# Kernel tuning notes

Measured on AMD Instinct MI355X. Metric: run time of the kernel, lower is better.

## Reference

```python
import jax, jax.numpy as jnp
import numpy as np

N = 50000          # number of nodes / output rows (len(degs))
IN_C, OUT_C = 16, 16
EDGE_F = 13        # edge feature dim fed to filter net
HID = 32           # filter-net hidden width
E_NOMINAL = 800000 # target number of edges (sum of degs)


def setup_inputs() -> dict:
    rng = np.random.default_rng(0)
    # variable per-node degrees in [0, 32], adjusted so they sum exactly to E_NOMINAL
    degs = rng.integers(0, 33, size=N).astype(np.int64)
    degs[0] = max(0, degs[0] + (E_NOMINAL - int(degs.sum())))
    E = int(degs.sum())
    # segment id of each edge = destination node (equivalent to the degs-driven loop)
    idxd = np.repeat(np.arange(N, dtype=np.int32), degs)
    idxn = rng.integers(0, N, size=E).astype(np.int32)  # source node gather index

    key = jax.random.key(0)
    k1, k2, k3, k4 = jax.random.split(key, 4)
    x = jax.random.normal(k1, (N, IN_C), jnp.float32)
    edgefeats = jax.random.normal(k2, (E, EDGE_F), jnp.float32)
    # filter net: Linear(EDGE_F->HID) -> ReLU -> Linear(HID->IN_C*OUT_C)
    W1 = jax.random.normal(k3, (EDGE_F, HID), jnp.float32) / np.float32(np.sqrt(EDGE_F))
    b1 = jnp.zeros((HID,), jnp.float32)
    W2 = jax.random.normal(k4, (HID, IN_C * OUT_C), jnp.float32) / np.float32(np.sqrt(HID))
    b2 = jnp.zeros((IN_C * OUT_C,), jnp.float32)
    return {
        "x": x, "edgefeats": edgefeats,
        "W1": W1, "b1": b1, "W2": W2, "b2": b2,
        "idxn": jnp.asarray(idxn), "idxd": jnp.asarray(idxd),
        "degs": jnp.asarray(degs.astype(np.float32)),
    }


def reference(x, edgefeats, W1, b1, W2, b2, idxn, idxd, degs):
    # filter net generates a per-edge [IN_C, OUT_C] weight matrix
    h = jax.nn.relu(edgefeats @ W1 + b1)                 # [E, HID]
    w = (h @ W2 + b2).reshape(-1, IN_C, OUT_C)           # [E, IN_C, OUT_C]
    # gather source-node features and apply per-edge matvec (bmm with [E,1,IN_C])
    sel = x[idxn]                                        # [E, IN_C]
    prod = jnp.einsum('ei,eio->eo', sel, w)              # [E, OUT_C]
    # segment-mean over each node's incoming edges; degree-0 nodes -> 0
    s = jax.ops.segment_sum(prod, idxd, num_segments=N)  # [N, OUT_C]
    d = degs[:, None]
    return jnp.where(d > 0, s / jnp.maximum(d, 1.0), jnp.float32(0.0))
```

## Files before the change

kernel.cpp:

```cpp
#include <hip/hip_runtime.h>

typedef _Float16 half2v __attribute__((ext_vector_type(2)));
typedef _Float16 half4v __attribute__((ext_vector_type(4)));
typedef _Float16 half8v __attribute__((ext_vector_type(8)));
typedef float   float4v __attribute__((ext_vector_type(4)));

#define INC     16
#define OUTC    16
#define EFN     13
#define HIDC    32
#define EPB     128
#define MAXSPAN 80

union H8 { half8v v; half2v h2[4]; };

__global__ __launch_bounds__(256) void prep(
    const float* __restrict__ W2,
    const float* __restrict__ x,
    _Float16*    __restrict__ wsB,
    _Float16*    __restrict__ wsXh,
    int nh)
{
    const int b = blockIdx.x;
    if (b < 32) {
        const int i = b * 256 + threadIdx.x;
        const int j = i & 7;
        const int l = (i >> 3) & 63;
        const int t = i >> 9;
        const int q = l >> 4, n = l & 15;
        const int kk = (j < 4) ? (q * 4 + j) : (16 + q * 4 + (j & 3));
        wsB[i] = (_Float16)W2[kk * 256 + t * 16 + n];
    } else {
        const int i = (b - 32) * 256 + threadIdx.x;
        if (i * 8 < nh) {
            const float4 v0 = ((const float4*)x)[i * 2];
            const float4 v1 = ((const float4*)x)[i * 2 + 1];
            half8v h;
            h[0] = (_Float16)v0.x; h[1] = (_Float16)v0.y;
            h[2] = (_Float16)v0.z; h[3] = (_Float16)v0.w;
            h[4] = (_Float16)v1.x; h[5] = (_Float16)v1.y;
            h[6] = (_Float16)v1.z; h[7] = (_Float16)v1.w;
            *(half8v*)(wsXh + (size_t)i * 8) = h;
        }
    }
}

__global__ __launch_bounds__(64, 4) void edge_kernel(
    const _Float16* __restrict__ xh,
    const float* __restrict__ edgefeats,
    const float* __restrict__ W1,
    const float* __restrict__ b1,
    const float* __restrict__ b2,
    const int*   __restrict__ idxn,
    const int*   __restrict__ idxd,
    const float* __restrict__ degs,
    const _Float16* __restrict__ wsB,
    float*       __restrict__ out,
    float*       __restrict__ wsPfirst,
    float*       __restrict__ wsPlast,
    int*         __restrict__ wsMeta,
    int E)
{
    __shared__ float lacc[MAXSPAN * OUTC];
    __shared__ __align__(4) unsigned char su[EPB];

    const int lane = threadIdx.x;
    const int n    = lane & 15;
    const int q    = lane >> 4;

    const long b0   = (long)blockIdx.x * EPB;
    const long bEnd = (b0 + EPB < (long)E) ? (b0 + EPB) : (long)E;
    const int  d_lo = idxd[b0];
    const int  d_hi = idxd[bEnd - 1];
    const int  span = d_hi - d_lo;

    H8 bfr[16];
    #pragma unroll
    for (int t = 0; t < 16; ++t)
        bfr[t].v = *(const half8v*)(wsB + ((size_t)(t * 64 + lane) * 8));

    #pragma unroll
    for (int it = 0; it < MAXSPAN * OUTC / 64; ++it) lacc[lane + it * 64] = 0.0f;
    {
        const int i2 = lane * 2;
        long e0 = b0 + i2, e1 = b0 + i2 + 1;
        if (e0 >= (long)E) e0 = E - 1;
        if (e1 >= (long)E) e1 = E - 1;
        const unsigned u0 = (unsigned)(idxd[e0] - d_lo);
        const unsigned u1 = (unsigned)(idxd[e1] - d_lo);
        *(unsigned short*)&su[i2] = (unsigned short)(u0 | (u1 << 8));
    }

    half4v a1, a2;
    float4v c1, c2;
    #pragma unroll
    for (int jj = 0; jj < 4; ++jj) {
        const int f = q * 4 + jj;
        const bool ok = (f < EFN);
        a1[jj] = ok ? (_Float16)W1[f * HIDC + n]      : (_Float16)0.f;
        a2[jj] = ok ? (_Float16)W1[f * HIDC + 16 + n] : (_Float16)0.f;
        c1[jj] = b1[q * 4 + jj];
        c2[jj] = b1[16 + q * 4 + jj];
    }
    half8v bfragB2;
    #pragma unroll
    for (int j = 0; j < 8; ++j) {
        _Float16 val = (_Float16)0.f;
        if (q < 2) val = (_Float16)b2[(q * 8 + j) * 16 + n];
        bfragB2[j] = val;
    }

    const int f0 = (q < 3) ? (q * 4) : 9;

    __syncthreads();

    const int ntile_blk = (int)((bEnd - b0 + 15) >> 4);

    const long Em1 = (long)E - 1;
    long e0n = b0 + n;
    const int node0 = idxn[(e0n < (long)E) ? e0n : Em1];
    int nodeN = idxn[(e0n + 16 < (long)E) ? (e0n + 16) : Em1];
    half8v xA = *(const half8v*)(xh + (size_t)node0 * INC);
    half8v xB = *(const half8v*)(xh + (size_t)node0 * INC + 8);
    long ec0 = (e0n < (long)E) ? e0n : Em1;
    float4 efc = *(const float4*)(edgefeats + (size_t)ec0 * EFN + f0);

    for (int t16 = 0; t16 < ntile_blk; ++t16) {
        const long base = b0 + (long)t16 * 16;
        const bool vM   = (base + n < (long)E);

        const long en2 = base + 32 + n;
        const int nodeN2 = idxn[(en2 < (long)E) ? en2 : Em1];
        const half8v xA1 = *(const half8v*)(xh + (size_t)nodeN * INC);
        const half8v xB1 = *(const half8v*)(xh + (size_t)nodeN * INC + 8);
        const long en1 = base + 16 + n;
        const long en1c = (en1 < (long)E) ? en1 : Em1;
        const float4 ef1 = *(const float4*)(edgefeats + (size_t)en1c * EFN + f0);

        const unsigned u4 = *(const unsigned*)&su[t16 * 16 + q * 4];

        H8 sa, sb_;
        sa.v = xA; sb_.v = xB;
        const half2v zz = {(_Float16)0.f, (_Float16)0.f};
        half2v selh[8];
        #pragma unroll
        for (int i = 0; i < 4; ++i) {
            selh[i]     = vM ? sa.h2[i]  : zz;
            selh[4 + i] = vM ? sb_.h2[i] : zz;
        }

        half4v efB;
        if (q < 3) {
            efB[0] = (_Float16)efc.x; efB[1] = (_Float16)efc.y;
            efB[2] = (_Float16)efc.z; efB[3] = (_Float16)efc.w;
        } else {
            efB[0] = (_Float16)efc.w; efB[1] = (_Float16)0.f;
            efB[2] = (_Float16)0.f;   efB[3] = (_Float16)0.f;
        }

        const float4v hf1 = __builtin_amdgcn_mfma_f32_16x16x16f16(a1, efB, c1, 0, 0, 0);
        const float4v hf2 = __builtin_amdgcn_mfma_f32_16x16x16f16(a2, efB, c2, 0, 0, 0);

        H8 hu;
        #pragma unroll
        for (int r = 0; r < 2; ++r) {
            half2v t1 = {(_Float16)fmaxf(hf1[2*r], 0.f), (_Float16)fmaxf(hf1[2*r+1], 0.f)};
            half2v t2 = {(_Float16)fmaxf(hf2[2*r], 0.f), (_Float16)fmaxf(hf2[2*r+1], 0.f)};
            hu.h2[r]     = t1;
            hu.h2[2 + r] = t2;
        }

        float4v acc = {0.f, 0.f, 0.f, 0.f};
        #pragma unroll
        for (int t = 0; t < 16; ++t) {
            _Float16 sv = (t & 1) ? selh[t >> 1][1] : selh[t >> 1][0];
            half2v sb = {sv, sv};
            H8 a;
            a.h2[0] = sb * hu.h2[0];
            a.h2[1] = sb * hu.h2[1];
            a.h2[2] = sb * hu.h2[2];
            a.h2[3] = sb * hu.h2[3];
            acc = __builtin_amdgcn_mfma_f32_16x16x32_f16(a.v, bfr[t].v, acc, 0, 0, 0);
        }
        {
            H8 a;
            #pragma unroll
            for (int j2 = 0; j2 < 4; ++j2) {
                a.h2[j2] = (q < 2) ? selh[q * 4 + j2] : zz;
            }
            acc = __builtin_amdgcn_mfma_f32_16x16x32_f16(a.v, bfragB2, acc, 0, 0, 0);
        }

        const unsigned rep = (u4 & 0xffu) * 0x01010101u;
        if (u4 == rep) {
            atomicAdd(&lacc[(u4 & 0xffu) * OUTC + n],
                      acc[0] + acc[1] + acc[2] + acc[3]);
        } else {
            #pragma unroll
            for (int r = 0; r < 4; ++r)
                atomicAdd(&lacc[((u4 >> (8 * r)) & 0xffu) * OUTC + n], acc[r]);
        }

        nodeN = nodeN2;
        xA = xA1; xB = xB1;
        efc = ef1;
    }

    __syncthreads();

    const bool first_starts = (b0 == 0)        || (idxd[b0 - 1] != d_lo);
    const bool last_ends    = (bEnd == (long)E) || (idxd[bEnd]   != d_hi);

    for (int i = lane; i < (span + 1) * OUTC; i += 64) {
        const int u = i >> 4;
        const int o = i & 15;
        const int v = d_lo + u;
        const float bin = lacc[u * OUTC + o];
        const bool starts = (u > 0)    || first_starts;
        const bool ends   = (u < span) || last_ends;
        if (starts && ends) {
            const float dg = degs[v];
            out[(size_t)v * OUTC + o] = (dg > 0.0f) ? bin / dg : 0.0f;
        } else if (!starts) {
            wsPfirst[(size_t)blockIdx.x * OUTC + o] = bin;
        } else {
            wsPlast[(size_t)blockIdx.x * OUTC + o] = bin;
        }
    }
    if (lane == 0) {
        wsMeta[blockIdx.x * 4 + 0] = d_hi;
        wsMeta[blockIdx.x * 4 + 1] = last_ends ? 1 : 0;
        wsMeta[blockIdx.x * 4 + 2] =
            (((span > 0) || first_starts) && !last_ends) ? 1 : 0;
    }
}

__global__ __launch_bounds__(256) void fixup_kernel(
    const float* __restrict__ degs,
    float*       __restrict__ out,
    const float* __restrict__ wsPfirst,
    const float* __restrict__ wsPlast,
    const int*   __restrict__ wsMeta,
    int N, int nblocks)
{
    const int t = blockIdx.x * 256 + threadIdx.x;

    if (t < nblocks && wsMeta[t * 4 + 2]) {
        const int v = wsMeta[t * 4 + 0];
        float tot[OUTC];
        #pragma unroll
        for (int o = 0; o < OUTC; ++o) tot[o] = wsPlast[(size_t)t * OUTC + o];
        for (int j = t + 1; j < nblocks; ++j) {
            #pragma unroll
            for (int o = 0; o < OUTC; ++o) tot[o] += wsPfirst[(size_t)j * OUTC + o];
            if (wsMeta[j * 4 + 0] != v || wsMeta[j * 4 + 1]) break;
        }
        const float dg = degs[v];
        #pragma unroll
        for (int o = 0; o < OUTC; ++o) out[(size_t)v * OUTC + o] = tot[o] / dg;
    }

    if (t < N && degs[t] == 0.0f) {
        float4* op = (float4*)(out + (size_t)t * OUTC);
        const float4 z = make_float4(0, 0, 0, 0);
        op[0] = z; op[1] = z; op[2] = z; op[3] = z;
    }
}

extern "C" void kernel_launch(void* const* d_in, const int* in_sizes, int n_in,
                              void* d_out, int out_size, void* d_ws, size_t ws_size,
                              hipStream_t stream)
{
    const float* x         = (const float*)d_in[0];
    const float* edgefeats = (const float*)d_in[1];
    const float* W1        = (const float*)d_in[2];
    const float* b1        = (const float*)d_in[3];
    const float* W2        = (const float*)d_in[4];
    const float* b2        = (const float*)d_in[5];
    const int*   idxn      = (const int*)d_in[6];
    const int*   idxd      = (const int*)d_in[7];
    const float* degs      = (const float*)d_in[8];

    const int E = in_sizes[6];
    const int N = in_sizes[8];
    const int nblocks = (E + EPB - 1) / EPB;
    const int nh = N * INC;

    _Float16* wsB  = (_Float16*)d_ws;
    _Float16* wsXh = (_Float16*)((char*)d_ws + 16384);
    size_t xh_bytes = ((size_t)nh * 2 + 255) & ~(size_t)255;
    float* wsPfirst = (float*)((char*)d_ws + 16384 + xh_bytes);
    float* wsPlast  = wsPfirst + (size_t)nblocks * OUTC;
    int*   wsMeta   = (int*)(wsPlast + (size_t)nblocks * OUTC);

    const int xhblocks = (nh / 8 + 255) / 256;
    prep<<<32 + xhblocks, 256, 0, stream>>>(W2, x, wsB, wsXh, nh);

    edge_kernel<<<nblocks, 64, 0, stream>>>(wsXh, edgefeats, W1, b1, b2,
                                            idxn, idxd, degs, wsB, (float*)d_out,
                                            wsPfirst, wsPlast, wsMeta, E);

    const int fthreads = (N > nblocks) ? N : nblocks;
    fixup_kernel<<<(fthreads + 255) / 256, 256, 0, stream>>>(
        degs, (float*)d_out, wsPfirst, wsPlast, wsMeta, N, nblocks);
}
```

Baseline: 167.8 us.

## Prefetch all tile edge features and indices upfront, double-buffer x gathers

All eight tiles' edge-feature float4s and source-node indices are loaded into registers at kernel start, before the weight-fragment loads and shared-memory init, so their latency overlaps that setup. The tile loop is fully unrolled to a fixed 8 iterations, and x gathers are double-buffered two tiles ahead with sched_barriers keeping the issue order. Occupancy hint drops from 4 to 3 waves to make room for the extra registers. Out-of-range edges in the last block are handled by the existing vM mask.

```diff
diff --git a/kernel.cpp b/kernel.cpp
--- a/kernel.cpp
+++ b/kernel.cpp
@@ -45,7 +45,7 @@
     }
 }
 
-__global__ __launch_bounds__(64, 4) void edge_kernel(
+__global__ __launch_bounds__(64, 3) void edge_kernel(
     const _Float16* __restrict__ xh,
     const float* __restrict__ edgefeats,
     const float* __restrict__ W1,
@@ -74,6 +74,24 @@
     const int  d_hi = idxd[bEnd - 1];
     const int  span = d_hi - d_lo;
 
+    const long Em1 = (long)E - 1;
+    const int  f0  = (q < 3) ? (q * 4) : 9;
+
+    float4 efr[8];
+    #pragma unroll
+    for (int t = 0; t < 8; ++t) {
+        long e = b0 + t * 16 + n;
+        if (e > Em1) e = Em1;
+        efr[t] = *(const float4*)(edgefeats + (size_t)e * EFN + f0);
+    }
+
+    int node[8];
+    #pragma unroll
+    for (int t = 0; t < 8; ++t) {
+        long e = b0 + t * 16 + n;
+        node[t] = idxn[(e <= Em1) ? e : Em1];
+    }
+
     H8 bfr[16];
     #pragma unroll
     for (int t = 0; t < 16; ++t)
@@ -84,8 +102,8 @@
     {
         const int i2 = lane * 2;
         long e0 = b0 + i2, e1 = b0 + i2 + 1;
-        if (e0 >= (long)E) e0 = E - 1;
-        if (e1 >= (long)E) e1 = E - 1;
+        if (e0 > Em1) e0 = Em1;
+        if (e1 > Em1) e1 = Em1;
         const unsigned u0 = (unsigned)(idxd[e0] - d_lo);
         const unsigned u1 = (unsigned)(idxd[e1] - d_lo);
         *(unsigned short*)&su[i2] = (unsigned short)(u0 | (u1 << 8));
@@ -110,32 +128,28 @@
         bfragB2[j] = val;
     }
 
-    const int f0 = (q < 3) ? (q * 4) : 9;
-
     __syncthreads();
 
-    const int ntile_blk = (int)((bEnd - b0 + 15) >> 4);
-
-    const long Em1 = (long)E - 1;
-    long e0n = b0 + n;
-    const int node0 = idxn[(e0n < (long)E) ? e0n : Em1];
-    int nodeN = idxn[(e0n + 16 < (long)E) ? (e0n + 16) : Em1];
-    half8v xA = *(const half8v*)(xh + (size_t)node0 * INC);
-    half8v xB = *(const half8v*)(xh + (size_t)node0 * INC + 8);
-    long ec0 = (e0n < (long)E) ? e0n : Em1;
-    float4 efc = *(const float4*)(edgefeats + (size_t)ec0 * EFN + f0);
-
-    for (int t16 = 0; t16 < ntile_blk; ++t16) {
+    half8v pxa[2], pxb[2];
+    pxa[0] = *(const half8v*)(xh + (size_t)node[0] * INC);
+    pxb[0] = *(const half8v*)(xh + (size_t)node[0] * INC + 8);
+    pxa[1] = *(const half8v*)(xh + (size_t)node[1] * INC);
+    pxb[1] = *(const half8v*)(xh + (size_t)node[1] * INC + 8);
+    __builtin_amdgcn_sched_barrier(0);
+
+    #pragma unroll
+    for (int t16 = 0; t16 < 8; ++t16) {
+        const int cur = t16 & 1;
         const long base = b0 + (long)t16 * 16;
         const bool vM   = (base + n < (long)E);
 
-        const long en2 = base + 32 + n;
-        const int nodeN2 = idxn[(en2 < (long)E) ? en2 : Em1];
-        const half8v xA1 = *(const half8v*)(xh + (size_t)nodeN * INC);
-        const half8v xB1 = *(const half8v*)(xh + (size_t)nodeN * INC + 8);
-        const long en1 = base + 16 + n;
-        const long en1c = (en1 < (long)E) ? en1 : Em1;
-        const float4 ef1 = *(const float4*)(edgefeats + (size_t)en1c * EFN + f0);
+        const half8v xA = pxa[cur];
+        const half8v xB = pxb[cur];
+        if (t16 + 2 < 8) {
+            pxa[cur] = *(const half8v*)(xh + (size_t)node[t16 + 2] * INC);
+            pxb[cur] = *(const half8v*)(xh + (size_t)node[t16 + 2] * INC + 8);
+        }
+        __builtin_amdgcn_sched_barrier(0);
 
         const unsigned u4 = *(const unsigned*)&su[t16 * 16 + q * 4];
 
@@ -151,11 +165,11 @@
 
         half4v efB;
         if (q < 3) {
-            efB[0] = (_Float16)efc.x; efB[1] = (_Float16)efc.y;
-            efB[2] = (_Float16)efc.z; efB[3] = (_Float16)efc.w;
+            efB[0] = (_Float16)efr[t16].x; efB[1] = (_Float16)efr[t16].y;
+            efB[2] = (_Float16)efr[t16].z; efB[3] = (_Float16)efr[t16].w;
         } else {
-            efB[0] = (_Float16)efc.w; efB[1] = (_Float16)0.f;
-            efB[2] = (_Float16)0.f;   efB[3] = (_Float16)0.f;
+            efB[0] = (_Float16)efr[t16].w; efB[1] = (_Float16)0.f;
+            efB[2] = (_Float16)0.f;        efB[3] = (_Float16)0.f;
         }
 
         const float4v hf1 = __builtin_amdgcn_mfma_f32_16x16x16f16(a1, efB, c1, 0, 0, 0);
@@ -200,10 +214,6 @@
             for (int r = 0; r < 4; ++r)
                 atomicAdd(&lacc[((u4 >> (8 * r)) & 0xffu) * OUTC + n], acc[r]);
         }
-
-        nodeN = nodeN2;
-        xA = xA1; xB = xB1;
-        efc = ef1;
     }
 
     __syncthreads();
```

Result: slower. 184.6 us (+10.0%).
